# Optimization experiments

Measured on AMD Instinct MI355X. Metric: run time of the kernel, lower is better.

## Reference

```python
import jax, jax.numpy as jnp
import numpy as np

N_WIRES = 12
DEPTH = 4
IN_DIM = 256
BATCH = 4096


def _apply_rx(state, theta, wire, n):
    """Apply RX(theta) = [[cos(t/2), -i sin(t/2)], [-i sin(t/2), cos(t/2)]] on `wire`.
    state: (batch, 2^n) complex. theta: scalar or (batch,) float."""
    half = theta * 0.5
    c = jnp.reshape(jnp.cos(half), (-1, 1, 1))  # broadcasts for scalar or per-batch
    s = jnp.reshape(jnp.sin(half), (-1, 1, 1))
    L, R = 2 ** wire, 2 ** (n - wire - 1)
    st = state.reshape(-1, L, 2, R)
    a0, a1 = st[:, :, 0], st[:, :, 1]
    b0 = c * a0 - 1j * s * a1
    b1 = -1j * s * a0 + c * a1
    return jnp.stack([b0, b1], axis=2).reshape(state.shape)


def _apply_cnot_adj(state, ctrl, n):
    """CNOT with control=ctrl, target=ctrl+1 (adjacent wires)."""
    L, R = 2 ** ctrl, 2 ** (n - ctrl - 2)
    st = state.reshape(-1, L, 2, 2, R)
    c0 = st[:, :, 0]
    c1 = st[:, :, 1, ::-1]  # flip target bit when control=1
    return jnp.stack([c0, c1], axis=2).reshape(state.shape)


def _pauli_z_signs(n):
    idx = np.arange(2 ** n)
    # wire 0 is the most-significant bit (torchquantum convention)
    bits = (idx[:, None] >> (n - 1 - np.arange(n))[None, :]) & 1
    return (1.0 - 2.0 * bits).astype(np.float32)  # (2^n, n)


def setup_inputs() -> dict:
    key = jax.random.key(0)
    k1, k2, k3 = jax.random.split(key, 3)
    x = jax.random.normal(k1, (BATCH, IN_DIM), dtype=jnp.float32)
    W = jax.random.normal(k2, (N_WIRES, IN_DIM), dtype=jnp.float32)
    params = jax.random.normal(k3, (DEPTH, N_WIRES, 1), dtype=jnp.float32)
    return {"x": x, "W": W, "params": params}


def reference(x, W, params):
    n = W.shape[0]
    depth = params.shape[0]
    batch = x.shape[0]
    angles = x @ W.T  # (batch, n) -- nn.Linear without bias
    state = jnp.zeros((batch, 2 ** n), dtype=jnp.complex64).at[:, 0].set(1.0)
    # data-encoding RX layer (per-batch angles)
    for w in range(n):
        state = _apply_rx(state, angles[:, w], w, n)
    # variational layers: RX(params) then CNOT ladder
    for d in range(depth):
        for w in range(n):
            state = _apply_rx(state, params[d, w, 0], w, n)
        for w in range(n - 1):
            state = _apply_cnot_adj(state, w, n)
    probs = jnp.real(state * jnp.conj(state))  # (batch, 2^n)
    signs = jnp.asarray(_pauli_z_signs(n))     # (2^n, n)
    return probs @ signs  # <Z_w> per wire, (batch, n)
```

## Files before the change

### kernel.cpp

```cpp
#include <hip/hip_runtime.h>
#include <math.h>

#define N_WIRES 12
#define DEPTH   4
#define NGATES  48
#define IN_DIM  256
#define ROWS_PER_BLOCK 16
#define XSTRIDE 272

struct Tabs {
    unsigned gm[NGATES];
    bool     rel[N_WIRES][NGATES];
    unsigned chi[NGATES];
    unsigned comp[N_WIRES];
};
constexpr int cparity(unsigned v) { int c = 0; while (v) { c ^= (int)(v & 1u); v >>= 1; } return c; }
constexpr Tabs make_tabs() {
    Tabs tb{};
    for (int g = 0; g < NGATES; ++g) {
        int d = g / N_WIRES, w = g % N_WIRES;
        unsigned m = 1u << w;
        if ((d == 1 || d == 3) && w + 1 < N_WIRES) m |= 1u << (w + 1);
        if ((d == 2 || d == 3) && w + 2 < N_WIRES) m |= 1u << (w + 2);
        if (d == 3 && w + 3 < N_WIRES)             m |= 1u << (w + 3);
        tb.gm[g] = m;
        unsigned c = 0;
        for (int i = 0; i < 16; ++i) c |= (unsigned)cparity(m & 0xFu & (unsigned)i) << i;
        tb.chi[g] = c;
    }
    for (int w = 0; w < N_WIRES; ++w) {
        unsigned S = (1u << w) | (w >= 4 ? (1u << (w - 4)) : 0u) | (w >= 8 ? (1u << (w - 8)) : 0u);
        for (int g = 0; g < NGATES; ++g) tb.rel[w][g] = cparity(tb.gm[g] & S) != 0;
        unsigned lc = (w < 4) ? 0u
                    : (w < 8) ? (1u << (w - 4))
                    : ((1u << (w - 8)) | ((w - 4 < 6) ? (1u << (w - 4)) : 0u));
        tb.comp[w] = 0x3Fu & ~lc;
    }
    return tb;
}
constexpr Tabs TB = make_tabs();

__global__ __launch_bounds__(256)
void fused_kernel(const float* __restrict__ x, const float* __restrict__ W,
                  const float* __restrict__ params, float* __restrict__ out)
{
    __shared__ float xl[ROWS_PER_BLOCK * XSTRIDE];
    __shared__ float wl[N_WIRES * IN_DIM];
    __shared__ float al[ROWS_PER_BLOCK * N_WIRES];
    __shared__ float tab[N_WIRES * 16];
    const int t = threadIdx.x;
    const int lane = t & 63;
    const int rowbase = blockIdx.x * ROWS_PER_BLOCK;

    if (t < N_WIRES * 16) tab[t] = 0.f;

    const float4* x4 = (const float4*)(x + (size_t)rowbase * IN_DIM);
    float4 xr[4];
    #pragma unroll
    for (int j = 0; j < 4; ++j) xr[j] = x4[t + 256 * j];
    const float4* W4 = (const float4*)W;
    float4 wr[3];
    #pragma unroll
    for (int j = 0; j < 3; ++j) wr[j] = W4[t + 256 * j];

    __syncthreads();

    float th[NGATES];
    #pragma unroll
    for (int g = 0; g < NGATES; ++g) {
        unsigned hs = (unsigned)(__popc((TB.gm[g] >> 4) & (unsigned)t) & 1);
        th[g] = __int_as_float(__float_as_int(params[g]) ^ (int)(hs << 31));
    }

    float P0[N_WIRES];
    #pragma unroll
    for (int w = 0; w < N_WIRES; ++w) {
        float p = 0.f;
        #pragma unroll
        for (int g = 0; g < NGATES; ++g)
            if (TB.rel[w][g] && (TB.gm[g] & 0xFu) == 0u) p += th[g];
        P0[w] = p;
    }

    float ca[N_WIRES][2], sa[N_WIRES][2];
    #pragma unroll
    for (int w = 0; w < N_WIRES; ++w)
        ca[w][0] = ca[w][1] = sa[w][0] = sa[w][1] = 0.f;
    #pragma unroll
    for (int i = 0; i < 16; ++i) {
        #pragma unroll
        for (int w = 0; w < N_WIRES; ++w) {
            float p = P0[w];
            #pragma unroll
            for (int g = 0; g < NGATES; ++g) {
                if (TB.rel[w][g] && (TB.gm[g] & 0xFu) != 0u) {
                    if ((TB.chi[g] >> i) & 1u) p -= th[g]; else p += th[g];
                }
            }
            float sn, cs;
            __sincosf(p, &sn, &cs);
            const int b = (i >> (w & 3)) & 1;
            ca[w][b] += cs; sa[w][b] += sn;
        }
    }

    #pragma unroll
    for (int w = 0; w < N_WIRES; ++w) {
        const unsigned comp = TB.comp[w];
        float v0c = ca[w][0], v1c = ca[w][1], v0s = sa[w][0], v1s = sa[w][1];
        #pragma unroll
        for (int d = 0; d < 6; ++d) {
            if (comp & (1u << d)) {
                v0c += __shfl_xor(v0c, 1 << d, 64);
                v1c += __shfl_xor(v1c, 1 << d, 64);
                v0s += __shfl_xor(v0s, 1 << d, 64);
                v1s += __shfl_xor(v1s, 1 << d, 64);
            }
        }
        if ((unsigned)(lane & (int)comp) == 0u) {
            unsigned fk = 0;
            if (w >= 4 && w < 8) fk = ((unsigned)t >> (w - 4)) & 1u;
            if (w >= 8) fk = (((unsigned)t >> (w - 8)) & 1u)
                           | ((((unsigned)t >> (w - 4)) & 1u) << 1);
            atomicAdd(&tab[w * 16 + (int)(fk << 1)],         v0c);
            atomicAdd(&tab[w * 16 + (int)(fk << 1) + 1],     v1c);
            atomicAdd(&tab[w * 16 + 8 + (int)(fk << 1)],     v0s);
            atomicAdd(&tab[w * 16 + 8 + (int)(fk << 1) + 1], v1s);
        }
    }

    #pragma unroll
    for (int j = 0; j < 4; ++j) {
        int f = t + 256 * j, row = f >> 6, c4 = f & 63;
        *(float4*)&xl[row * XSTRIDE + c4 * 4] = xr[j];
    }
    #pragma unroll
    for (int j = 0; j < 3; ++j) ((float4*)wl)[t + 256 * j] = wr[j];
    __syncthreads();

    const int r = t >> 4, p = t & 15;
    float partial[N_WIRES];
    #pragma unroll
    for (int w = 0; w < N_WIRES; ++w) partial[w] = 0.f;
    for (int i2 = 0; i2 < 16; ++i2) {
        float xv = xl[r * XSTRIDE + i2 * 16 + p];
        #pragma unroll
        for (int w = 0; w < N_WIRES; ++w)
            partial[w] = fmaf(xv, wl[w * IN_DIM + i2 * 16 + p], partial[w]);
    }
    #pragma unroll
    for (int w = 0; w < N_WIRES; ++w) {
        float v = partial[w];
        v += __shfl_xor(v, 1, 16);
        v += __shfl_xor(v, 2, 16);
        v += __shfl_xor(v, 4, 16);
        v += __shfl_xor(v, 8, 16);
        partial[w] = v;
    }
    if (p < N_WIRES) al[r * N_WIRES + p] = partial[p];
    __syncthreads();

    if (t < ROWS_PER_BLOCK * N_WIRES) {
        const int r2 = t / N_WIRES;
        const int w  = t - r2 * N_WIRES;
        const int nb = 1 + (w >= 4) + (w >= 8);
        const float a0 = al[r2 * N_WIRES + (w & 3)];
        const float a1 = (w >= 4) ? al[r2 * N_WIRES + ((w >= 8) ? (w - 4) : w)] : 0.f;
        const float a2 = (w >= 8) ? al[r2 * N_WIRES + w] : 0.f;
        float o = 0.f;
        const int nk = 1 << nb;
        for (int kap = 0; kap < nk; ++kap) {
            float B = (kap & 1) ? -a0 : a0;
            if (nb > 1) B += (kap & 2) ? -a1 : a1;
            if (nb > 2) B += (kap & 4) ? -a2 : a2;
            float sn, cs;
            __sincosf(B, &sn, &cs);
            o = fmaf(cs,  tab[w * 16 + kap],     o);
            o = fmaf(-sn, tab[w * 16 + 8 + kap], o);
        }
        out[(size_t)(rowbase + r2) * N_WIRES + w] = o * (1.f / 4096.f);
    }
}

extern "C" void kernel_launch(void* const* d_in, const int* in_sizes, int n_in,
                              void* d_out, int out_size, void* d_ws, size_t ws_size,
                              hipStream_t stream) {
    const float* x      = (const float*)d_in[0];
    const float* W      = (const float*)d_in[1];
    const float* params = (const float*)d_in[2];
    float* out          = (float*)d_out;
    (void)d_ws; (void)ws_size;

    const int batch = in_sizes[0] / IN_DIM;
    hipLaunchKernelGGL(fused_kernel, dim3(batch / ROWS_PER_BLOCK), dim3(256), 0, stream,
                       x, W, params, out);
}
```

Measured before the change: 71.23 us.

## Split batch-independent table computation into separate small kernel

The parameter-only trig table was previously recomputed redundantly by every one of the 256 blocks, each doing 16×12 sincos per thread plus shuffles and atomics. This moves it into a 16-block precompute kernel that writes partial tables to workspace, and the main kernel sums the 16 partials per entry. It removes redundant per-block compute at the cost of an extra launch and a global round trip through the workspace.

```diff
diff --git a/kernel.cpp b/kernel.cpp
--- a/kernel.cpp
+++ b/kernel.cpp
@@ -7,6 +7,7 @@
 #define IN_DIM  256
 #define ROWS_PER_BLOCK 16
 #define XSTRIDE 272
+#define TABSZ   (N_WIRES * 16)
 
 struct Tabs {
     unsigned gm[NGATES];
@@ -41,18 +42,71 @@
 constexpr Tabs TB = make_tabs();
 
 __global__ __launch_bounds__(256)
-void fused_kernel(const float* __restrict__ x, const float* __restrict__ W,
-                  const float* __restrict__ params, float* __restrict__ out)
+void tab_kernel(const float* __restrict__ params, float* __restrict__ ws)
+{
+    __shared__ float tab[TABSZ];
+    const int t = threadIdx.x;
+    const int lane = t & 63;
+    const unsigned i = blockIdx.x;
+
+    if (t < TABSZ) tab[t] = 0.f;
+    __syncthreads();
+
+    float th[NGATES];
+    #pragma unroll
+    for (int g = 0; g < NGATES; ++g) {
+        unsigned hs = (unsigned)(__popc((TB.gm[g] >> 4) & (unsigned)t) & 1);
+        hs ^= (TB.chi[g] >> i) & 1u;
+        th[g] = __int_as_float(__float_as_int(params[g]) ^ (int)(hs << 31));
+    }
+
+    float ca[N_WIRES], sa[N_WIRES];
+    #pragma unroll
+    for (int w = 0; w < N_WIRES; ++w) {
+        float p = 0.f;
+        #pragma unroll
+        for (int g = 0; g < NGATES; ++g)
+            if (TB.rel[w][g]) p += th[g];
+        float sn, cs;
+        __sincosf(p, &sn, &cs);
+        ca[w] = cs; sa[w] = sn;
+    }
+
+    #pragma unroll
+    for (int w = 0; w < N_WIRES; ++w) {
+        const unsigned comp = TB.comp[w];
+        float vc = ca[w], vs = sa[w];
+        #pragma unroll
+        for (int d = 0; d < 6; ++d) {
+            if (comp & (1u << d)) {
+                vc += __shfl_xor(vc, 1 << d, 64);
+                vs += __shfl_xor(vs, 1 << d, 64);
+            }
+        }
+        if ((unsigned)(lane & (int)comp) == 0u) {
+            unsigned fk = 0;
+            if (w >= 4 && w < 8) fk = ((unsigned)t >> (w - 4)) & 1u;
+            if (w >= 8) fk = (((unsigned)t >> (w - 8)) & 1u)
+                           | ((((unsigned)t >> (w - 4)) & 1u) << 1);
+            const int b = (int)((i >> (w & 3)) & 1u);
+            atomicAdd(&tab[w * 16 + (int)(fk << 1) + b],     vc);
+            atomicAdd(&tab[w * 16 + 8 + (int)(fk << 1) + b], vs);
+        }
+    }
+    __syncthreads();
+    if (t < TABSZ) ws[(int)i * TABSZ + t] = tab[t];
+}
+
+__global__ __launch_bounds__(256)
+void main_kernel(const float* __restrict__ x, const float* __restrict__ W,
+                 const float* __restrict__ tabg, float* __restrict__ out)
 {
     __shared__ float xl[ROWS_PER_BLOCK * XSTRIDE];
     __shared__ float wl[N_WIRES * IN_DIM];
     __shared__ float al[ROWS_PER_BLOCK * N_WIRES];
-    __shared__ float tab[N_WIRES * 16];
+    __shared__ float tab[TABSZ];
     const int t = threadIdx.x;
-    const int lane = t & 63;
     const int rowbase = blockIdx.x * ROWS_PER_BLOCK;
-
-    if (t < N_WIRES * 16) tab[t] = 0.f;
 
     const float4* x4 = (const float4*)(x + (size_t)rowbase * IN_DIM);
     float4 xr[4];
@@ -63,70 +117,11 @@
     #pragma unroll
     for (int j = 0; j < 3; ++j) wr[j] = W4[t + 256 * j];
 
-    __syncthreads();
-
-    float th[NGATES];
-    #pragma unroll
-    for (int g = 0; g < NGATES; ++g) {
-        unsigned hs = (unsigned)(__popc((TB.gm[g] >> 4) & (unsigned)t) & 1);
-        th[g] = __int_as_float(__float_as_int(params[g]) ^ (int)(hs << 31));
-    }
-
-    float P0[N_WIRES];
-    #pragma unroll
-    for (int w = 0; w < N_WIRES; ++w) {
-        float p = 0.f;
+    if (t < TABSZ) {
+        float s = 0.f;
         #pragma unroll
-        for (int g = 0; g < NGATES; ++g)
-            if (TB.rel[w][g] && (TB.gm[g] & 0xFu) == 0u) p += th[g];
-        P0[w] = p;
-    }
-
-    float ca[N_WIRES][2], sa[N_WIRES][2];
-    #pragma unroll
-    for (int w = 0; w < N_WIRES; ++w)
-        ca[w][0] = ca[w][1] = sa[w][0] = sa[w][1] = 0.f;
-    #pragma unroll
-    for (int i = 0; i < 16; ++i) {
-        #pragma unroll
-        for (int w = 0; w < N_WIRES; ++w) {
-            float p = P0[w];
-            #pragma unroll
-            for (int g = 0; g < NGATES; ++g) {
-                if (TB.rel[w][g] && (TB.gm[g] & 0xFu) != 0u) {
-                    if ((TB.chi[g] >> i) & 1u) p -= th[g]; else p += th[g];
-                }
-            }
-            float sn, cs;
-            __sincosf(p, &sn, &cs);
-            const int b = (i >> (w & 3)) & 1;
-            ca[w][b] += cs; sa[w][b] += sn;
-        }
-    }
-
-    #pragma unroll
-    for (int w = 0; w < N_WIRES; ++w) {
-        const unsigned comp = TB.comp[w];
-        float v0c = ca[w][0], v1c = ca[w][1], v0s = sa[w][0], v1s = sa[w][1];
-        #pragma unroll
-        for (int d = 0; d < 6; ++d) {
-            if (comp & (1u << d)) {
-                v0c += __shfl_xor(v0c, 1 << d, 64);
-                v1c += __shfl_xor(v1c, 1 << d, 64);
-                v0s += __shfl_xor(v0s, 1 << d, 64);
-                v1s += __shfl_xor(v1s, 1 << d, 64);
-            }
-        }
-        if ((unsigned)(lane & (int)comp) == 0u) {
-            unsigned fk = 0;
-            if (w >= 4 && w < 8) fk = ((unsigned)t >> (w - 4)) & 1u;
-            if (w >= 8) fk = (((unsigned)t >> (w - 8)) & 1u)
-                           | ((((unsigned)t >> (w - 4)) & 1u) << 1);
-            atomicAdd(&tab[w * 16 + (int)(fk << 1)],         v0c);
-            atomicAdd(&tab[w * 16 + (int)(fk << 1) + 1],     v1c);
-            atomicAdd(&tab[w * 16 + 8 + (int)(fk << 1)],     v0s);
-            atomicAdd(&tab[w * 16 + 8 + (int)(fk << 1) + 1], v1s);
-        }
+        for (int ii = 0; ii < 16; ++ii) s += tabg[ii * TABSZ + t];
+        tab[t] = s;
     }
 
     #pragma unroll
@@ -189,9 +184,11 @@
     const float* W      = (const float*)d_in[1];
     const float* params = (const float*)d_in[2];
     float* out          = (float*)d_out;
-    (void)d_ws; (void)ws_size;
+    float* ws           = (float*)d_ws;
 
     const int batch = in_sizes[0] / IN_DIM;
-    hipLaunchKernelGGL(fused_kernel, dim3(batch / ROWS_PER_BLOCK), dim3(256), 0, stream,
-                       x, W, params, out);
+    hipLaunchKernelGGL(tab_kernel,  dim3(16),                     dim3(256), 0, stream,
+                       params, ws);
+    hipLaunchKernelGGL(main_kernel, dim3(batch / ROWS_PER_BLOCK), dim3(256), 0, stream,
+                       x, W, ws, out);
 }
```

Result: faster. 66.41 us (-6.8%).
